# Performance work log

Hardware: AMD Instinct MI355X
Metric: run time of the kernel (lower is better)

## Reference

```python
import jax, jax.numpy as jnp
import numpy as np

QMAX = 127.0  # torch.iinfo(torch.int8).max


def setup_inputs() -> dict:
    key = jax.random.key(0)
    k1, k2 = jax.random.split(key)
    input_act = jax.random.normal(k1, (4, 2048, 4096), dtype=jnp.float32)
    # nn.Linear weight: [out_features, in_features], fp weights pre-quantization
    weight = jax.random.normal(k2, (4096, 4096), dtype=jnp.float32) * 0.02
    return {"input_act": input_act, "weight": weight}


def reference(input_act, weight):
    # --- weight_quant (per-channel over in_features) ---
    w_scale = jnp.max(jnp.abs(weight), axis=-1, keepdims=True) / QMAX      # [O, 1]
    w_q = jnp.round(weight / w_scale).astype(jnp.int8)                      # int8 weight

    # --- activation quant (per-token over last dim) ---
    a_scale = jnp.max(jnp.abs(input_act), axis=-1, keepdims=True) / QMAX    # [B, S, 1]
    x_q = jnp.round(input_act / a_scale).astype(jnp.int8)                   # int8 acts

    # --- int8 GEMM with int32 accumulation (torch._int_mm semantics) ---
    # [B, S, K] @ [K, O] -> [B, S, O]
    acc = jnp.matmul(x_q.astype(jnp.int32), w_q.T.astype(jnp.int32))        # exact int32

    # --- dequant: scale = input_act_scale * weight_scale.T, then cast to fp16 ---
    scale = a_scale * w_scale.T[None, :, :]                                 # [B, S, O]
    out = (acc.astype(jnp.float32) * scale).astype(jnp.float16)
    return out
```

## Files before the change

### kernel.cpp

```cpp
#include <hip/hip_runtime.h>
#include <hip/hip_fp16.h>
#include <cstdint>

typedef int v4i __attribute__((ext_vector_type(4)));

#define AS1C(p) ((const __attribute__((address_space(1))) void*)(p))
#define AS3(p)  ((__attribute__((address_space(3))) void*)(p))

__global__ __launch_bounds__(256) void quant_rows(const float* __restrict__ X,
                                                  int8_t* __restrict__ Q,
                                                  float* __restrict__ scales,
                                                  int K) {
    const int row = blockIdx.x;
    const float4* xv = (const float4*)(X + (size_t)row * K);

    float4 v[4];
#pragma unroll
    for (int j = 0; j < 4; ++j) v[j] = xv[threadIdx.x + (j << 8)];

    float m = 0.0f;
#pragma unroll
    for (int j = 0; j < 4; ++j) {
        m = fmaxf(m, fmaxf(fmaxf(fabsf(v[j].x), fabsf(v[j].y)),
                           fmaxf(fabsf(v[j].z), fabsf(v[j].w))));
    }
    for (int off = 32; off > 0; off >>= 1)
        m = fmaxf(m, __shfl_xor(m, off, 64));

    __shared__ float wmax[4];
    __shared__ float s_sc;
    const int lane = threadIdx.x & 63;
    const int wv = threadIdx.x >> 6;
    if (lane == 0) wmax[wv] = m;
    __syncthreads();
    if (threadIdx.x == 0) {
        float mm = fmaxf(fmaxf(wmax[0], wmax[1]), fmaxf(wmax[2], wmax[3]));
        float sc = mm / 127.0f;
        scales[row] = sc;
        s_sc = sc;
    }
    __syncthreads();
    const float sc = s_sc;

    char4* qv = (char4*)(Q + (size_t)row * K);
#pragma unroll
    for (int j = 0; j < 4; ++j) {
        char4 q;
        q.x = (signed char)(int)rintf(v[j].x / sc);
        q.y = (signed char)(int)rintf(v[j].y / sc);
        q.z = (signed char)(int)rintf(v[j].z / sc);
        q.w = (signed char)(int)rintf(v[j].w / sc);
        qv[threadIdx.x + (j << 8)] = q;
    }
}

__global__ __launch_bounds__(512, 2) void gemm_i8(const int8_t* __restrict__ Aq,
                                                  const int8_t* __restrict__ Bq,
                                                  const float* __restrict__ a_scale,
                                                  const float* __restrict__ w_scale,
                                                  float* __restrict__ out) {
    extern __shared__ __align__(16) int8_t smem[];

    const int K = 4096;
    const int bid = blockIdx.x;
    const int wg  = (bid & 7) * 64 + (bid >> 3);
    const int n0 = (wg & 15) * 256;
    const int m0 = (wg >> 4) * 256;

    const int tid  = threadIdx.x;
    const int lane = tid & 63;
    const int wid  = tid >> 6;
    const int wm   = wid >> 2;
    const int wn   = wid & 3;

    const int rsel  = lane & 15;
    const int kswz  = ((lane >> 4) << 4) ^ (((rsel >> 1) & 3) << 4);
    const int abase = (wm * 128 + rsel) * 64 + kswz;
    const int bbase = 16384 + (wn * 64 + rsel) * 64 + kswz;

    const int strow = tid >> 2;
    const int stswz = ((strow >> 1) & 3) << 4;
    const int stcol = ((tid & 3) << 4) ^ stswz;
    const int8_t* gA = Aq + (size_t)(m0 + strow) * K + stcol;
    const int8_t* gB = Bq + (size_t)(n0 + strow) * K + stcol;
    const size_t rstep = (size_t)128 * K;
    const int ldsst = wid * 1024;

    v4i acc[8][4] = {};
    v4i aFa[8], aFb[8], bFa[4], bFb[4];

#define STAGE(buf, kt) do {                                                          \
    int8_t* _d = smem + (buf) * 32768;                                               \
    const int8_t* _a = gA + (size_t)(kt) * 64;                                       \
    const int8_t* _b = gB + (size_t)(kt) * 64;                                       \
    __builtin_amdgcn_global_load_lds(AS1C(_a),         AS3(_d + ldsst),         16, 0, 0); \
    __builtin_amdgcn_global_load_lds(AS1C(_a + rstep), AS3(_d + 8192  + ldsst), 16, 0, 0); \
    __builtin_amdgcn_global_load_lds(AS1C(_b),         AS3(_d + 16384 + ldsst), 16, 0, 0); \
    __builtin_amdgcn_global_load_lds(AS1C(_b + rstep), AS3(_d + 24576 + ldsst), 16, 0, 0); \
  } while (0)

#define GROUP(g, CA, CB, NA, NB, gsrc, goff)  do {                                   \
    NA[2*(g)]     = *(const v4i*)(bufN + abase + (2*(g))     * 1024);                \
    NA[2*(g) + 1] = *(const v4i*)(bufN + abase + (2*(g) + 1) * 1024);                \
    NB[(g)]       = *(const v4i*)(bufN + bbase + (g) * 1024);                        \
    __builtin_amdgcn_global_load_lds(AS1C(gsrc), AS3(pD + (goff) + ldsst), 16, 0, 0);\
    __builtin_amdgcn_sched_barrier(0);                                               \
    __builtin_amdgcn_s_setprio(1);                                                   \
    _Pragma("unroll")                                                                \
    for (int nt = 0; nt < 4; ++nt) {                                                 \
        acc[2*(g)][nt] = __builtin_amdgcn_mfma_i32_16x16x64_i8(                      \
            CA[2*(g)], CB[nt], acc[2*(g)][nt], 0, 0, 0);                             \
        acc[2*(g)+1][nt] = __builtin_amdgcn_mfma_i32_16x16x64_i8(                    \
            CA[2*(g)+1], CB[nt], acc[2*(g)+1][nt], 0, 0, 0);                         \
    }                                                                                \
    __builtin_amdgcn_s_setprio(0);                                                   \
    __builtin_amdgcn_sched_barrier(0);                                               \
  } while (0)

#define KSTEP(u, CA, CB, NA, NB, kt4) do {                                           \
    const int kt  = (kt4) + (u);                                                     \
    const int8_t* bufN = smem + (((u) + 1) & 3) * 32768;                             \
    int8_t* pD = smem + (((u) + 3) & 3) * 32768;                                     \
    const int ktp = (kt + 3 < 64) ? (kt + 3) : 63;                                   \
    const int8_t* _a = gA + (size_t)ktp * 64;                                        \
    const int8_t* _b = gB + (size_t)ktp * 64;                                        \
    asm volatile("s_waitcnt vmcnt(4)" ::: "memory");                                 \
    __builtin_amdgcn_s_barrier();                                                    \
    GROUP(0, CA, CB, NA, NB, _a,         0);                                         \
    GROUP(1, CA, CB, NA, NB, _a + rstep, 8192);                                      \
    GROUP(2, CA, CB, NA, NB, _b,         16384);                                     \
    GROUP(3, CA, CB, NA, NB, _b + rstep, 24576);                                     \
  } while (0)

    STAGE(0, 0); STAGE(1, 1); STAGE(2, 2);
    asm volatile("s_waitcnt vmcnt(8)" ::: "memory");
    __builtin_amdgcn_s_barrier();
#pragma unroll
    for (int mt = 0; mt < 8; ++mt) aFa[mt] = *(const v4i*)(smem + abase + mt * 1024);
#pragma unroll
    for (int nt = 0; nt < 4; ++nt) bFa[nt] = *(const v4i*)(smem + bbase + nt * 1024);

    for (int kt4 = 0; kt4 < 64; kt4 += 4) {
        KSTEP(0, aFa, bFa, aFb, bFb, kt4);
        KSTEP(1, aFb, bFb, aFa, bFa, kt4);
        KSTEP(2, aFa, bFa, aFb, bFb, kt4);
        KSTEP(3, aFb, bFb, aFa, bFa, kt4);
    }

    const int r0  = (lane >> 4) << 2;
    const int col = lane & 15;
#pragma unroll
    for (int mt = 0; mt < 8; ++mt) {
        const int tbase = m0 + wm * 128 + mt * 16 + r0;
        float as[4];
#pragma unroll
        for (int r = 0; r < 4; ++r) as[r] = a_scale[tbase + r];
#pragma unroll
        for (int nt = 0; nt < 4; ++nt) {
            const int o = n0 + wn * 64 + nt * 16 + col;
            const float wsc = w_scale[o];
#pragma unroll
            for (int r = 0; r < 4; ++r) {
                float v = (float)acc[mt][nt][r] * as[r] * wsc;
                out[(size_t)(tbase + r) * 4096 + o] = __half2float(__float2half_rn(v));
            }
        }
    }
#undef KSTEP
#undef GROUP
#undef STAGE
}

extern "C" void kernel_launch(void* const* d_in, const int* in_sizes, int n_in,
                              void* d_out, int out_size, void* d_ws, size_t ws_size,
                              hipStream_t stream) {
    const float* input_act = (const float*)d_in[0];
    const float* weight    = (const float*)d_in[1];
    float* out = (float*)d_out;

    const int K = 4096, O = 4096, T = 8192;

    int8_t* x_q = (int8_t*)d_ws;
    int8_t* w_q = x_q + (size_t)T * K;
    float* a_scale = (float*)(w_q + (size_t)O * K);
    float* w_scale = a_scale + T;

    static bool attr_done = false;
    if (!attr_done) {
        hipFuncSetAttribute(reinterpret_cast<const void*>(gemm_i8),
                            hipFuncAttributeMaxDynamicSharedMemorySize, 131072);
        attr_done = true;
    }

    quant_rows<<<T, 256, 0, stream>>>(input_act, x_q, a_scale, K);
    quant_rows<<<O, 256, 0, stream>>>(weight, w_q, w_scale, K);

    dim3 grid(512);
    gemm_i8<<<grid, 512, 131072, stream>>>(x_q, w_q, a_scale, w_scale, out);
}
```

Before: 180.4 us.

## Load B fragments directly from global memory and fuse the two quant kernels

The GEMM stops staging the weight tile through LDS. Each wave now reads its B fragments straight from global memory into registers one k-step ahead, which halves LDS use and allows full vmcnt(0) waits instead of finer-grained ones. The two quantization launches are merged into one grid covering both activation and weight rows, saving a launch. The trade-off is that B is now read redundantly per wave from global/L2 with exposed latency, and the finer-grained interleaving of global_load_lds with MFMA groups is lost.

```diff
diff --git a/kernel.cpp b/kernel.cpp
--- a/kernel.cpp
+++ b/kernel.cpp
@@ -7,12 +7,23 @@
 #define AS1C(p) ((const __attribute__((address_space(1))) void*)(p))
 #define AS3(p)  ((__attribute__((address_space(3))) void*)(p))
 
-__global__ __launch_bounds__(256) void quant_rows(const float* __restrict__ X,
-                                                  int8_t* __restrict__ Q,
-                                                  float* __restrict__ scales,
-                                                  int K) {
+__global__ __launch_bounds__(256) void quant_fused(const float* __restrict__ X,
+                                                   const float* __restrict__ W,
+                                                   int8_t* __restrict__ Xq,
+                                                   int8_t* __restrict__ Wq,
+                                                   float* __restrict__ a_scale,
+                                                   float* __restrict__ w_scale) {
     const int row = blockIdx.x;
-    const float4* xv = (const float4*)(X + (size_t)row * K);
+    const float* src;
+    int8_t* dst;
+    float* scp;
+    if (row < 8192) {
+        src = X + (size_t)row * 4096;  dst = Xq + (size_t)row * 4096;  scp = a_scale + row;
+    } else {
+        const int r = row - 8192;
+        src = W + (size_t)r * 4096;    dst = Wq + (size_t)r * 4096;    scp = w_scale + r;
+    }
+    const float4* xv = (const float4*)src;
 
     float4 v[4];
 #pragma unroll
@@ -36,13 +47,13 @@
     if (threadIdx.x == 0) {
         float mm = fmaxf(fmaxf(wmax[0], wmax[1]), fmaxf(wmax[2], wmax[3]));
         float sc = mm / 127.0f;
-        scales[row] = sc;
+        *scp = sc;
         s_sc = sc;
     }
     __syncthreads();
     const float sc = s_sc;
 
-    char4* qv = (char4*)(Q + (size_t)row * K);
+    char4* qv = (char4*)dst;
 #pragma unroll
     for (int j = 0; j < 4; ++j) {
         char4 q;
@@ -74,15 +85,16 @@
     const int wn   = wid & 3;
 
     const int rsel  = lane & 15;
-    const int kswz  = ((lane >> 4) << 4) ^ (((rsel >> 1) & 3) << 4);
+    const int koff  = (lane >> 4) << 4;
+    const int kswz  = koff ^ (((rsel >> 1) & 3) << 4);
     const int abase = (wm * 128 + rsel) * 64 + kswz;
-    const int bbase = 16384 + (wn * 64 + rsel) * 64 + kswz;
+
+    const int8_t* pB = Bq + (size_t)(n0 + wn * 64 + rsel) * K + koff;
 
     const int strow = tid >> 2;
     const int stswz = ((strow >> 1) & 3) << 4;
     const int stcol = ((tid & 3) << 4) ^ stswz;
     const int8_t* gA = Aq + (size_t)(m0 + strow) * K + stcol;
-    const int8_t* gB = Bq + (size_t)(n0 + strow) * K + stcol;
     const size_t rstep = (size_t)128 * K;
     const int ldsst = wid * 1024;
 
@@ -90,55 +102,50 @@
     v4i aFa[8], aFb[8], bFa[4], bFb[4];
 
 #define STAGE(buf, kt) do {                                                          \
-    int8_t* _d = smem + (buf) * 32768;                                               \
+    int8_t* _d = smem + (buf) * 16384;                                               \
     const int8_t* _a = gA + (size_t)(kt) * 64;                                       \
-    const int8_t* _b = gB + (size_t)(kt) * 64;                                       \
-    __builtin_amdgcn_global_load_lds(AS1C(_a),         AS3(_d + ldsst),         16, 0, 0); \
-    __builtin_amdgcn_global_load_lds(AS1C(_a + rstep), AS3(_d + 8192  + ldsst), 16, 0, 0); \
-    __builtin_amdgcn_global_load_lds(AS1C(_b),         AS3(_d + 16384 + ldsst), 16, 0, 0); \
-    __builtin_amdgcn_global_load_lds(AS1C(_b + rstep), AS3(_d + 24576 + ldsst), 16, 0, 0); \
-  } while (0)
-
-#define GROUP(g, CA, CB, NA, NB, gsrc, goff)  do {                                   \
-    NA[2*(g)]     = *(const v4i*)(bufN + abase + (2*(g))     * 1024);                \
-    NA[2*(g) + 1] = *(const v4i*)(bufN + abase + (2*(g) + 1) * 1024);                \
-    NB[(g)]       = *(const v4i*)(bufN + bbase + (g) * 1024);                        \
-    __builtin_amdgcn_global_load_lds(AS1C(gsrc), AS3(pD + (goff) + ldsst), 16, 0, 0);\
-    __builtin_amdgcn_sched_barrier(0);                                               \
-    __builtin_amdgcn_s_setprio(1);                                                   \
-    _Pragma("unroll")                                                                \
-    for (int nt = 0; nt < 4; ++nt) {                                                 \
-        acc[2*(g)][nt] = __builtin_amdgcn_mfma_i32_16x16x64_i8(                      \
-            CA[2*(g)], CB[nt], acc[2*(g)][nt], 0, 0, 0);                             \
-        acc[2*(g)+1][nt] = __builtin_amdgcn_mfma_i32_16x16x64_i8(                    \
-            CA[2*(g)+1], CB[nt], acc[2*(g)+1][nt], 0, 0, 0);                         \
-    }                                                                                \
-    __builtin_amdgcn_s_setprio(0);                                                   \
-    __builtin_amdgcn_sched_barrier(0);                                               \
+    __builtin_amdgcn_global_load_lds(AS1C(_a),         AS3(_d + ldsst),        16, 0, 0); \
+    __builtin_amdgcn_global_load_lds(AS1C(_a + rstep), AS3(_d + 8192 + ldsst), 16, 0, 0); \
   } while (0)
 
 #define KSTEP(u, CA, CB, NA, NB, kt4) do {                                           \
     const int kt  = (kt4) + (u);                                                     \
-    const int8_t* bufN = smem + (((u) + 1) & 3) * 32768;                             \
-    int8_t* pD = smem + (((u) + 3) & 3) * 32768;                                     \
+    const int8_t* bufN = smem + (((u) + 1) & 3) * 16384;                             \
     const int ktp = (kt + 3 < 64) ? (kt + 3) : 63;                                   \
-    const int8_t* _a = gA + (size_t)ktp * 64;                                        \
-    const int8_t* _b = gB + (size_t)ktp * 64;                                        \
-    asm volatile("s_waitcnt vmcnt(4)" ::: "memory");                                 \
+    const int ktb = (kt + 1 < 64) ? (kt + 1) : 63;                                   \
+    const int8_t* _pb = pB + (size_t)ktb * 64;                                       \
+    asm volatile("s_waitcnt vmcnt(0)" ::: "memory");           \
     __builtin_amdgcn_s_barrier();                                                    \
-    GROUP(0, CA, CB, NA, NB, _a,         0);                                         \
-    GROUP(1, CA, CB, NA, NB, _a + rstep, 8192);                                      \
-    GROUP(2, CA, CB, NA, NB, _b,         16384);                                     \
-    GROUP(3, CA, CB, NA, NB, _b + rstep, 24576);                                     \
+    STAGE(((u) + 3) & 3, ktp);                                                       \
+    NB[0] = *(const v4i*)(_pb);                                                      \
+    NB[1] = *(const v4i*)(_pb + (size_t)16 * K);                                     \
+    NB[2] = *(const v4i*)(_pb + (size_t)32 * K);                                     \
+    NB[3] = *(const v4i*)(_pb + (size_t)48 * K);                                     \
+    _Pragma("unroll")                                                                \
+    for (int g = 0; g < 4; ++g) {                                                    \
+        NA[2*g]     = *(const v4i*)(bufN + abase + (2*g)     * 1024);                \
+        NA[2*g + 1] = *(const v4i*)(bufN + abase + (2*g + 1) * 1024);                \
+        __builtin_amdgcn_s_setprio(1);                                               \
+        _Pragma("unroll")                                                            \
+        for (int nt = 0; nt < 4; ++nt) {                                             \
+            acc[2*g][nt] = __builtin_amdgcn_mfma_i32_16x16x64_i8(                    \
+                CA[2*g], CB[nt], acc[2*g][nt], 0, 0, 0);                             \
+            acc[2*g+1][nt] = __builtin_amdgcn_mfma_i32_16x16x64_i8(                  \
+                CA[2*g+1], CB[nt], acc[2*g+1][nt], 0, 0, 0);                         \
+        }                                                                            \
+        __builtin_amdgcn_s_setprio(0);                                               \
+    }                                                                                \
   } while (0)
 
     STAGE(0, 0); STAGE(1, 1); STAGE(2, 2);
-    asm volatile("s_waitcnt vmcnt(8)" ::: "memory");
+    bFa[0] = *(const v4i*)(pB);
+    bFa[1] = *(const v4i*)(pB + (size_t)16 * K);
+    bFa[2] = *(const v4i*)(pB + (size_t)32 * K);
+    bFa[3] = *(const v4i*)(pB + (size_t)48 * K);
+    asm volatile("s_waitcnt vmcnt(0)" ::: "memory");
     __builtin_amdgcn_s_barrier();
 #pragma unroll
     for (int mt = 0; mt < 8; ++mt) aFa[mt] = *(const v4i*)(smem + abase + mt * 1024);
-#pragma unroll
-    for (int nt = 0; nt < 4; ++nt) bFa[nt] = *(const v4i*)(smem + bbase + nt * 1024);
 
     for (int kt4 = 0; kt4 < 64; kt4 += 4) {
         KSTEP(0, aFa, bFa, aFb, bFb, kt4);
@@ -167,7 +174,6 @@
         }
     }
 #undef KSTEP
-#undef GROUP
 #undef STAGE
 }
 
@@ -188,13 +194,13 @@
     static bool attr_done = false;
     if (!attr_done) {
         hipFuncSetAttribute(reinterpret_cast<const void*>(gemm_i8),
-                            hipFuncAttributeMaxDynamicSharedMemorySize, 131072);
+                            hipFuncAttributeMaxDynamicSharedMemorySize, 65536);
         attr_done = true;
     }
 
-    quant_rows<<<T, 256, 0, stream>>>(input_act, x_q, a_scale, K);
-    quant_rows<<<O, 256, 0, stream>>>(weight, w_q, w_scale, K);
+    quant_fused<<<T + O, 256, 0, stream>>>(input_act, weight, x_q, w_q,
+                                           a_scale, w_scale);
 
     dim3 grid(512);
-    gemm_i8<<<grid, 512, 131072, stream>>>(x_q, w_q, a_scale, w_scale, out);
+    gemm_i8<<<grid, 512, 65536, stream>>>(x_q, w_q, a_scale, w_scale, out);
 }
```

Result: slower. 253.0 us (+40.2%).
